# Performance work log

Measured on AMD Instinct MI355X. Metric: run time of the kernel, lower is better.

The kernel has to match this reference:

```python
import jax, jax.numpy as jnp
import numpy as np

N = 100000   # nodes
E = 1600000  # edges
D = 128      # input feature dim
H = 128      # hidden dim
C = 40       # output classes


def _gcn_conv(x, W, b, src, dst, norm):
    # PyG GCNConv: h = x @ W; out_i = sum_j (d_i^-1/2 d_j^-1/2) h_j over in-edges,
    # including self-loops, then + bias. norm = deg^-1/2 with self-loop-augmented degree.
    h = x @ W                                    # [N, H]
    coef = norm[src] * norm[dst]                 # [E]
    agg = jax.ops.segment_sum(h[src] * coef[:, None], dst, num_segments=N)
    agg = agg + h * (norm * norm)[:, None]       # self-loop term
    return agg + b


def setup_inputs() -> dict:
    key = jax.random.key(0)
    ks = jax.random.split(key, 12)
    x = jax.random.normal(ks[0], (N, D), dtype=jnp.float32)
    edge_index = jax.random.randint(ks[1], (2, E), 0, N, dtype=jnp.int64)

    def lin(k, fan_in, fan_out):
        s = 1.0 / np.sqrt(fan_in)
        return jax.random.uniform(k, (fan_in, fan_out), jnp.float32, -s, s)

    return {
        "x": x,
        "edge_index": edge_index,
        "W1": lin(ks[2], D, H), "b1": jnp.zeros((H,), jnp.float32),
        "W2": lin(ks[3], H, H), "b2": jnp.zeros((H,), jnp.float32),
        "W3": lin(ks[4], H, H), "b3": jnp.zeros((H,), jnp.float32),
        "Wp1": lin(ks[5], H, H), "bp1": jnp.zeros((H,), jnp.float32),
        "Wp2": lin(ks[6], H, C), "bp2": jnp.zeros((C,), jnp.float32),
    }


def reference(x, edge_index, W1, b1, W2, b2, W3, b3, Wp1, bp1, Wp2, bp2):
    src, dst = edge_index[0], edge_index[1]
    # degree with self-loops (GCNConv adds self-loops by default)
    deg = jax.ops.segment_sum(jnp.ones((E,), jnp.float32), dst, num_segments=N) + 1.0
    norm = jax.lax.rsqrt(deg)                    # deg^-1/2

    h = x
    for W, b in ((W1, b1), (W2, b2), (W3, b3)):
        h = _gcn_conv(h, W, b, src, dst, norm)
        h = jax.nn.relu(h)
        # dropout is a no-op at inference / rate 0

    h = h @ Wp1 + bp1
    h = h @ Wp2 + bp2
    return jax.nn.log_softmax(h, axis=1)
```

## Files before the change

### kernel.cpp

```cpp
#include <hip/hip_runtime.h>
#include <hip/hip_bf16.h>
#include <math.h>


#define DH 128
#define NC 40
#define BN 128
#define MAXNB 1024
#define CAP 2560
#define CH 4096
#define SP 136

typedef __attribute__((ext_vector_type(8))) short bf16x8;
typedef __attribute__((ext_vector_type(4))) float f32x4;

__device__ __forceinline__ unsigned short f2bf(float f) {
    unsigned u = __float_as_uint(f);
    unsigned r = (u + 0x7fffu + ((u >> 16) & 1u)) >> 16;
    return (unsigned short)r;
}
__device__ __forceinline__ unsigned pack2(float lo, float hi) {
    return (unsigned)f2bf(lo) | ((unsigned)f2bf(hi) << 16);
}


__global__ __launch_bounds__(256) void init_bpos(unsigned* __restrict__ bpos, int NB) {
    int i = blockIdx.x * 256 + threadIdx.x;
    if (i < NB) bpos[i] = (unsigned)i * CAP;
}


__global__ __launch_bounds__(256) void bucket_scatter(const int* __restrict__ src,
                                                      const int* __restrict__ dst, int E,
                                                      unsigned* __restrict__ bpos,
                                                      unsigned* __restrict__ ebuf) {
    __shared__ unsigned hist[MAXNB];
    __shared__ unsigned gbase[MAXNB];
    __shared__ unsigned lim[MAXNB];
    __shared__ unsigned cur[MAXNB];
    int tid = threadIdx.x;
    int e0 = blockIdx.x * CH;
    int nE = min(CH, E - e0);

    for (int i = tid; i < MAXNB; i += 256) { hist[i] = 0; cur[i] = 0; }
    __syncthreads();
    for (int i = tid; i < nE; i += 256)
        atomicAdd(&hist[(unsigned)dst[e0 + i] >> 7], 1u);
    __syncthreads();
    for (int i = tid; i < MAXNB; i += 256) {
        unsigned h = hist[i];
        if (h) {
            unsigned o = atomicAdd(&bpos[i], h);
            gbase[i] = o;
            lim[i] = min(o + h, (unsigned)(i + 1) * CAP);
        }
    }
    __syncthreads();
    for (int i = tid; i < nE; i += 256) {
        int s = src[e0 + i];
        int d = dst[e0 + i];
        unsigned b = (unsigned)d >> 7;
        unsigned p = gbase[b] + atomicAdd(&cur[b], 1u);
        if (p < lim[b]) ebuf[p] = ((unsigned)s << 7) | ((unsigned)d & 127u);
    }
}


__global__ __launch_bounds__(256) void bucket_degfill(const unsigned* __restrict__ ebuf,
                                                      const unsigned* __restrict__ bpos,
                                                      unsigned* __restrict__ cnt,
                                                      float* __restrict__ nrm,
                                                      unsigned* __restrict__ offN,
                                                      unsigned* __restrict__ dh,
                                                      int* __restrict__ csr, int N) {
    __shared__ unsigned h[BN], lb[BN], cur[BN];
    __shared__ int lcsr[CAP];
    __shared__ unsigned dhh[256];
    __shared__ unsigned tot;

    int b = blockIdx.x, tid = threadIdx.x;
    unsigned ebase = (unsigned)b * CAP;
    unsigned used = min(bpos[b] - ebase, (unsigned)CAP);

    if (tid < BN) { h[tid] = 0; cur[tid] = 0; }
    dhh[tid] = 0;
    if (tid == 0) tot = 0;
    __syncthreads();

    for (unsigned i = tid; i < used; i += 256)
        atomicAdd(&h[ebuf[ebase + i] & 127u], 1u);
    __syncthreads();

    if (tid < BN) {
        unsigned m = h[tid];
        lb[tid] = m ? atomicAdd(&tot, m) : 0u;
    }
    __syncthreads();

    for (unsigned i = tid; i < used; i += 256) {
        unsigned v = ebuf[ebase + i];
        unsigned nl = v & 127u;
        unsigned r = atomicAdd(&cur[nl], 1u);
        lcsr[lb[nl] + r] = (int)(v >> 7);
    }

    if (tid < BN) {
        int node = b * BN + tid;
        if (node < N) {
            unsigned m = h[tid];
            cnt[node] = m;
            nrm[node] = rsqrtf((float)m + 1.0f);
            offN[node] = ebase + lb[tid];
            atomicAdd(&dhh[min(m, 255u)], 1u);
        }
    }
    __syncthreads();

    for (unsigned i = tid; i < used; i += 256)
        csr[ebase + i] = lcsr[i];
    if (dhh[tid]) atomicAdd(&dh[tid], dhh[tid]);
}


__global__ __launch_bounds__(256) void deg_scatter(const unsigned* __restrict__ cnt, int N,
                                                   const unsigned* __restrict__ dh,
                                                   unsigned* __restrict__ binpos,
                                                   const unsigned* __restrict__ offN,
                                                   int* __restrict__ perm,
                                                   unsigned* __restrict__ pd2) {
    __shared__ unsigned hh[256], base[256], cur[256], sdh[256], sns[256];
    int t = threadIdx.x;
    hh[t] = 0; cur[t] = 0; sdh[t] = dh[t];
    __syncthreads();
    unsigned ns = 0;
    for (int d = t + 1; d < 256; ++d) ns += sdh[d];
    sns[t] = ns;
    int i = blockIdx.x * 256 + t;
    unsigned d = 0;
    if (i < N) { d = min(cnt[i], 255u); atomicAdd(&hh[d], 1u); }
    __syncthreads();
    if (hh[t]) base[t] = sns[t] + atomicAdd(&binpos[t], hh[t]);
    __syncthreads();
    if (i < N) {
        unsigned r = atomicAdd(&cur[d], 1u);
        unsigned idx = base[d] + r;
        perm[idx] = i;
        pd2[idx] = (offN[i] << 9) | min(cnt[i], 511u);
    }
}


__global__ __launch_bounds__(256) void prep_w(const float* __restrict__ W1,
                                              const float* __restrict__ W2,
                                              const float* __restrict__ W3,
                                              const float* __restrict__ Wp1,
                                              const float* __restrict__ bp1,
                                              const float* __restrict__ Wp2,
                                              const float* __restrict__ bp2,
                                              unsigned short* __restrict__ Wt,
                                              unsigned short* __restrict__ Wft,
                                              float* __restrict__ bfh) {
    int id = blockIdx.x * 256 + threadIdx.x;
    if (id < 3 * DH * DH) {
        int l = id >> 14, r = id & (DH * DH - 1);
        int k = r >> 7, n = r & 127;
        const float* W = (l == 0) ? W1 : (l == 1) ? W2 : W3;
        Wt[l * DH * DH + n * DH + k] = f2bf(W[k * DH + n]);
    } else if (id < 3 * DH * DH + 48 * DH) {
        int o = id - 3 * DH * DH;
        int c = o >> 7, k = o & 127;
        float acc = 0.f;
        if (c < NC)
            for (int j = 0; j < DH; ++j) acc += Wp1[k * DH + j] * Wp2[j * NC + c];
        Wft[c * DH + k] = f2bf(acc);
    } else if (id < 3 * DH * DH + 48 * DH + 48) {
        int c = id - 3 * DH * DH - 48 * DH;
        float acc = 0.f;
        if (c < NC) {
            acc = bp2[c];
            for (int j = 0; j < DH; ++j) acc += bp1[j] * Wp2[j * NC + c];
        }
        bfh[c] = acc;
    }
}


__global__ __launch_bounds__(256) void gemm_mfma_f32(const float* __restrict__ X,
                                                     const unsigned short* __restrict__ Wt,
                                                     const float* __restrict__ nrm,
                                                     unsigned short* __restrict__ outb,
                                                     int nrows) {
    const int tid = threadIdx.x;
    const int wave = tid >> 6;
    const int lane = tid & 63;
    const int m = lane & 15;
    const int quad = lane >> 4;
    const int rbase = blockIdx.x * 128 + wave * 32;

    union U8 { bf16x8 v; unsigned u[4]; };

    f32x4 acc[2][8];
#pragma unroll
    for (int rt = 0; rt < 2; ++rt)
#pragma unroll
        for (int ct = 0; ct < 8; ++ct) acc[rt][ct] = (f32x4){0.f, 0.f, 0.f, 0.f};

#pragma unroll
    for (int kt = 0; kt < 4; ++kt) {
        const int kof = kt * 32 + quad * 8;
        bf16x8 a[2], b[8];
#pragma unroll
        for (int rt = 0; rt < 2; ++rt) {
            int r = rbase + rt * 16 + m;
            r = (r < nrows) ? r : (nrows - 1);
            const float* p = X + (size_t)r * DH + kof;
            float4 u0 = *(const float4*)p;
            float4 u1 = *(const float4*)(p + 4);
            U8 t;
            t.u[0] = pack2(u0.x, u0.y);
            t.u[1] = pack2(u0.z, u0.w);
            t.u[2] = pack2(u1.x, u1.y);
            t.u[3] = pack2(u1.z, u1.w);
            a[rt] = t.v;
        }
#pragma unroll
        for (int ct = 0; ct < 8; ++ct)
            b[ct] = *(const bf16x8*)(Wt + (ct * 16 + m) * DH + kof);
#pragma unroll
        for (int rt = 0; rt < 2; ++rt)
#pragma unroll
            for (int ct = 0; ct < 8; ++ct)
                acc[rt][ct] = __builtin_amdgcn_mfma_f32_16x16x32_bf16(a[rt], b[ct], acc[rt][ct], 0, 0, 0);
    }

#pragma unroll
    for (int rt = 0; rt < 2; ++rt)
#pragma unroll
        for (int reg = 0; reg < 4; ++reg) {
            int r = rbase + rt * 16 + quad * 4 + reg;
            if (r < nrows) {
                float s = nrm[r];
#pragma unroll
                for (int ct = 0; ct < 8; ++ct)
                    outb[(size_t)r * DH + ct * 16 + m] = f2bf(acc[rt][ct][reg] * s);
            }
        }
}


__device__ __forceinline__ void bf8_add(float* acc, uint4 v) {
    acc[0] += __uint_as_float(v.x << 16);
    acc[1] += __uint_as_float(v.x & 0xffff0000u);
    acc[2] += __uint_as_float(v.y << 16);
    acc[3] += __uint_as_float(v.y & 0xffff0000u);
    acc[4] += __uint_as_float(v.z << 16);
    acc[5] += __uint_as_float(v.z & 0xffff0000u);
    acc[6] += __uint_as_float(v.w << 16);
    acc[7] += __uint_as_float(v.w & 0xffff0000u);
}

__device__ __forceinline__ void gather_phase(const uint4* __restrict__ Abf,
                                             const int* __restrict__ csr,
                                             const unsigned* __restrict__ pd2,
                                             const int* __restrict__ perm,
                                             const float* __restrict__ bias,
                                             unsigned short (*sA)[SP],
                                             int* snode, float* snrm, int N) {
    const int tid = threadIdx.x;
    const int g = tid >> 4;
    const int lane = tid & 15;
    const int idx = blockIdx.x * 16 + g;
    if (idx < N) {
        const unsigned pd = pd2[idx];
        const unsigned o = pd >> 9;
        const unsigned d = pd & 511u;
        const int node = perm[idx];

        float acc[8];
        {
            uint4 v = Abf[(size_t)node * 16 + lane];
            acc[0] = __uint_as_float(v.x << 16);
            acc[1] = __uint_as_float(v.x & 0xffff0000u);
            acc[2] = __uint_as_float(v.y << 16);
            acc[3] = __uint_as_float(v.y & 0xffff0000u);
            acc[4] = __uint_as_float(v.z << 16);
            acc[5] = __uint_as_float(v.z & 0xffff0000u);
            acc[6] = __uint_as_float(v.w << 16);
            acc[7] = __uint_as_float(v.w & 0xffff0000u);
        }

        unsigned e = 0;
        for (; e + 4 <= d; e += 4) {
            int s0 = csr[o + e + 0];
            int s1 = csr[o + e + 1];
            int s2 = csr[o + e + 2];
            int s3 = csr[o + e + 3];
            uint4 v0 = Abf[(size_t)s0 * 16 + lane];
            uint4 v1 = Abf[(size_t)s1 * 16 + lane];
            uint4 v2 = Abf[(size_t)s2 * 16 + lane];
            uint4 v3 = Abf[(size_t)s3 * 16 + lane];
            bf8_add(acc, v0);
            bf8_add(acc, v1);
            bf8_add(acc, v2);
            bf8_add(acc, v3);
        }
        for (; e < d; ++e) {
            int s = csr[o + e];
            uint4 v = Abf[(size_t)s * 16 + lane];
            bf8_add(acc, v);
        }

        float nm = rsqrtf((float)d + 1.0f);
        if (lane == 0) { snode[g] = node; snrm[g] = nm; }
        float4 b0 = *(const float4*)(bias + lane * 8);
        float4 b1 = *(const float4*)(bias + lane * 8 + 4);
        uint4 ov;
        ov.x = pack2(fmaxf(acc[0] * nm + b0.x, 0.f), fmaxf(acc[1] * nm + b0.y, 0.f));
        ov.y = pack2(fmaxf(acc[2] * nm + b0.z, 0.f), fmaxf(acc[3] * nm + b0.w, 0.f));
        ov.z = pack2(fmaxf(acc[4] * nm + b1.x, 0.f), fmaxf(acc[5] * nm + b1.y, 0.f));
        ov.w = pack2(fmaxf(acc[6] * nm + b1.z, 0.f), fmaxf(acc[7] * nm + b1.w, 0.f));
        *(uint4*)&sA[g][lane * 8] = ov;
    }
    __syncthreads();
}


__global__ __launch_bounds__(256) void agg_gemm(const uint4* __restrict__ Abf,
                                                const int* __restrict__ csr,
                                                const unsigned* __restrict__ pd2,
                                                const int* __restrict__ perm,
                                                const float* __restrict__ bias,
                                                const unsigned short* __restrict__ Wt,
                                                unsigned short* __restrict__ outb, int N) {
    __shared__ unsigned short sA[16][SP];
    __shared__ int snode[16];
    __shared__ float snrm[16];
    gather_phase(Abf, csr, pd2, perm, bias, sA, snode, snrm, N);

    const int tid = threadIdx.x;
    const int wave = tid >> 6;
    const int l64 = tid & 63;
    const int m = l64 & 15;
    const int quad = l64 >> 4;

    f32x4 acc[2];
    acc[0] = (f32x4){0.f, 0.f, 0.f, 0.f};
    acc[1] = (f32x4){0.f, 0.f, 0.f, 0.f};

#pragma unroll
    for (int kt = 0; kt < 4; ++kt) {
        const int kof = kt * 32 + quad * 8;
        bf16x8 a = *(const bf16x8*)&sA[m][kof];
#pragma unroll
        for (int c2 = 0; c2 < 2; ++c2) {
            const int ct = wave * 2 + c2;
            bf16x8 b = *(const bf16x8*)(Wt + (ct * 16 + m) * DH + kof);
            acc[c2] = __builtin_amdgcn_mfma_f32_16x16x32_bf16(a, b, acc[c2], 0, 0, 0);
        }
    }

#pragma unroll
    for (int reg = 0; reg < 4; ++reg) {
        int idx = blockIdx.x * 16 + quad * 4 + reg;
        if (idx < N) {
            int r = snode[quad * 4 + reg];
            float s = snrm[quad * 4 + reg];
#pragma unroll
            for (int c2 = 0; c2 < 2; ++c2)
                outb[(size_t)r * DH + (wave * 2 + c2) * 16 + m] = f2bf(acc[c2][reg] * s);
        }
    }
}


__global__ __launch_bounds__(256) void agg_head(const uint4* __restrict__ Abf,
                                                const int* __restrict__ csr,
                                                const unsigned* __restrict__ pd2,
                                                const int* __restrict__ perm,
                                                const float* __restrict__ bias,
                                                const unsigned short* __restrict__ Wft,
                                                const float* __restrict__ bfh,
                                                float* __restrict__ out, int N) {
    __shared__ unsigned short sA[16][SP];
    __shared__ int snode[16];
    __shared__ float snrm[16];
    gather_phase(Abf, csr, pd2, perm, bias, sA, snode, snrm, N);

    const int tid = threadIdx.x;
    if (tid >= 64) return;
    const int m = tid & 15;
    const int quad = tid >> 4;

    f32x4 acc[3];
#pragma unroll
    for (int ct = 0; ct < 3; ++ct) acc[ct] = (f32x4){0.f, 0.f, 0.f, 0.f};

#pragma unroll
    for (int kt = 0; kt < 4; ++kt) {
        const int kof = kt * 32 + quad * 8;
        bf16x8 a = *(const bf16x8*)&sA[m][kof];
#pragma unroll
        for (int ct = 0; ct < 3; ++ct) {
            bf16x8 b = *(const bf16x8*)(Wft + (ct * 16 + m) * DH + kof);
            acc[ct] = __builtin_amdgcn_mfma_f32_16x16x32_bf16(a, b, acc[ct], 0, 0, 0);
        }
    }

    float bias0 = bfh[m];
    float bias1 = bfh[16 + m];
    float bias2 = bfh[32 + m];

#pragma unroll
    for (int reg = 0; reg < 4; ++reg) {
        float v0 = acc[0][reg] + bias0;
        float v1 = acc[1][reg] + bias1;
        float v2 = (m < 8) ? (acc[2][reg] + bias2) : -1e30f;
        float mx = fmaxf(fmaxf(v0, v1), v2);
#pragma unroll
        for (int dlt = 1; dlt < 16; dlt <<= 1) mx = fmaxf(mx, __shfl_xor(mx, dlt));
        float s = __expf(v0 - mx) + __expf(v1 - mx) + ((m < 8) ? __expf(v2 - mx) : 0.f);
#pragma unroll
        for (int dlt = 1; dlt < 16; dlt <<= 1) s += __shfl_xor(s, dlt);
        float ls = mx + __logf(s);
        int idx = blockIdx.x * 16 + quad * 4 + reg;
        if (idx < N) {
            int r = snode[quad * 4 + reg];
            out[(size_t)r * NC + m] = v0 - ls;
            out[(size_t)r * NC + 16 + m] = v1 - ls;
            if (m < 8) out[(size_t)r * NC + 32 + m] = v2 - ls;
        }
    }
}


extern "C" void kernel_launch(void* const* d_in, const int* in_sizes, int n_in,
                              void* d_out, int out_size, void* d_ws, size_t ws_size,
                              hipStream_t stream) {
    const float* x   = (const float*)d_in[0];
    const int*   ei  = (const int*)d_in[1];
    const float* W1  = (const float*)d_in[2];
    const float* b1  = (const float*)d_in[3];
    const float* W2  = (const float*)d_in[4];
    const float* b2  = (const float*)d_in[5];
    const float* W3  = (const float*)d_in[6];
    const float* b3  = (const float*)d_in[7];
    const float* Wp1 = (const float*)d_in[8];
    const float* bp1 = (const float*)d_in[9];
    const float* Wp2 = (const float*)d_in[10];
    const float* bp2 = (const float*)d_in[11];
    float* out = (float*)d_out;

    const int N = in_sizes[0] / DH;
    const int E = in_sizes[1] / 2;
    const int* src = ei;
    const int* dst = ei + E;
    const int NB = (N + BN - 1) / BN;

    char* w = (char*)d_ws;
    unsigned short* Ab  = (unsigned short*)w; w += (size_t)N * DH * 2;
    unsigned short* Bb  = (unsigned short*)w; w += (size_t)N * DH * 2;
    int*      csr    = (int*)w;      w += (size_t)NB * CAP * 4;
    unsigned* ebuf   = (unsigned*)w; w += (size_t)NB * CAP * 4;
    unsigned* dh     = (unsigned*)w; w += 256 * 4;
    unsigned* binpos = (unsigned*)w; w += 256 * 4;
    unsigned* bpos   = (unsigned*)w; w += MAXNB * 4;
    unsigned* cnt    = (unsigned*)w; w += (size_t)N * 4;
    float*    nrm    = (float*)w;    w += (size_t)N * 4;
    unsigned* offN   = (unsigned*)w; w += (size_t)N * 4;
    unsigned* pd2    = (unsigned*)w; w += (size_t)((N + 31) & ~31) * 4;
    int*      perm   = (int*)w;      w += (size_t)((N + 31) & ~31) * 4;
    unsigned short* Wt  = (unsigned short*)w; w += 3 * DH * DH * 2;
    unsigned short* Wft = (unsigned short*)w; w += 48 * DH * 2;
    float*    bfh    = (float*)w;    w += 64 * 4;

    const int gC = (E + CH - 1) / CH;
    const int gN = (N + 255) / 256;

    hipMemsetAsync(dh, 0, 256 * 4 + 256 * 4, stream);
    init_bpos     <<<(NB + 255) / 256, 256, 0, stream>>>(bpos, NB);
    bucket_scatter<<<gC, 256, 0, stream>>>(src, dst, E, bpos, ebuf);
    bucket_degfill<<<NB, 256, 0, stream>>>(ebuf, bpos, cnt, nrm, offN, dh, csr, N);
    deg_scatter   <<<gN, 256, 0, stream>>>(cnt, N, dh, binpos, offN, perm, pd2);
    prep_w<<<(3 * DH * DH + 48 * DH + 48 + 255) / 256, 256, 0, stream>>>(
        W1, W2, W3, Wp1, bp1, Wp2, bp2, Wt, Wft, bfh);

    const int gG = (N + 127) / 128;
    const int gF = (N + 15) / 16;

    gemm_mfma_f32<<<gG, 256, 0, stream>>>(x, Wt, nrm, Ab, N);
    agg_gemm<<<gF, 256, 0, stream>>>((const uint4*)Ab, csr, pd2, perm, b1,
                                     Wt + DH * DH, Bb, N);
    agg_gemm<<<gF, 256, 0, stream>>>((const uint4*)Bb, csr, pd2, perm, b2,
                                     Wt + 2 * DH * DH, Ab, N);
    agg_head<<<gF, 256, 0, stream>>>((const uint4*)Ab, csr, pd2, perm, b3,
                                     Wft, bfh, out, N);
}
```

Baseline: 399.1 us.

## Vectorize bucketing loads, shuffle-broadcast CSR indices in gather, raise occupancy bounds

The bucket scatter and degree-fill kernels now read edge and bucket data as 128-bit vectors, and the CSR write-back is done in int4 chunks. In the gather phase, each 16-lane group loads up to 64 neighbor indices cooperatively and broadcasts them with shuffles, replacing the repeated scalar CSR loads per edge. Launch bounds on the aggregation kernels request 8 blocks per SM, which may push the compiler to limit registers. The aims are fewer memory transactions and more latency hiding, at the cost of shuffle overhead and possible register spills. The int4 loads also assume each chunk's base offset is 16-byte aligned.

```diff
diff --git a/kernel.cpp b/kernel.cpp
--- a/kernel.cpp
+++ b/kernel.cpp
@@ -41,10 +41,18 @@
     int tid = threadIdx.x;
     int e0 = blockIdx.x * CH;
     int nE = min(CH, E - e0);
+    int nE4 = nE & ~3;
 
     for (int i = tid; i < MAXNB; i += 256) { hist[i] = 0; cur[i] = 0; }
     __syncthreads();
-    for (int i = tid; i < nE; i += 256)
+    for (int i = tid * 4; i < nE4; i += 1024) {
+        int4 dv = *(const int4*)(dst + e0 + i);
+        atomicAdd(&hist[(unsigned)dv.x >> 7], 1u);
+        atomicAdd(&hist[(unsigned)dv.y >> 7], 1u);
+        atomicAdd(&hist[(unsigned)dv.z >> 7], 1u);
+        atomicAdd(&hist[(unsigned)dv.w >> 7], 1u);
+    }
+    for (int i = nE4 + tid; i < nE; i += 256)
         atomicAdd(&hist[(unsigned)dst[e0 + i] >> 7], 1u);
     __syncthreads();
     for (int i = tid; i < MAXNB; i += 256) {
@@ -56,7 +64,31 @@
         }
     }
     __syncthreads();
-    for (int i = tid; i < nE; i += 256) {
+    for (int i = tid * 4; i < nE4; i += 1024) {
+        int4 sv = *(const int4*)(src + e0 + i);
+        int4 dv = *(const int4*)(dst + e0 + i);
+        {
+            unsigned b = (unsigned)dv.x >> 7;
+            unsigned p = gbase[b] + atomicAdd(&cur[b], 1u);
+            if (p < lim[b]) ebuf[p] = ((unsigned)sv.x << 7) | ((unsigned)dv.x & 127u);
+        }
+        {
+            unsigned b = (unsigned)dv.y >> 7;
+            unsigned p = gbase[b] + atomicAdd(&cur[b], 1u);
+            if (p < lim[b]) ebuf[p] = ((unsigned)sv.y << 7) | ((unsigned)dv.y & 127u);
+        }
+        {
+            unsigned b = (unsigned)dv.z >> 7;
+            unsigned p = gbase[b] + atomicAdd(&cur[b], 1u);
+            if (p < lim[b]) ebuf[p] = ((unsigned)sv.z << 7) | ((unsigned)dv.z & 127u);
+        }
+        {
+            unsigned b = (unsigned)dv.w >> 7;
+            unsigned p = gbase[b] + atomicAdd(&cur[b], 1u);
+            if (p < lim[b]) ebuf[p] = ((unsigned)sv.w << 7) | ((unsigned)dv.w & 127u);
+        }
+    }
+    for (int i = nE4 + tid; i < nE; i += 256) {
         int s = src[e0 + i];
         int d = dst[e0 + i];
         unsigned b = (unsigned)d >> 7;
@@ -81,13 +113,21 @@
     int b = blockIdx.x, tid = threadIdx.x;
     unsigned ebase = (unsigned)b * CAP;
     unsigned used = min(bpos[b] - ebase, (unsigned)CAP);
+    unsigned used4 = used & ~3u;
 
     if (tid < BN) { h[tid] = 0; cur[tid] = 0; }
     dhh[tid] = 0;
     if (tid == 0) tot = 0;
     __syncthreads();
 
-    for (unsigned i = tid; i < used; i += 256)
+    for (unsigned i = tid * 4; i < used4; i += 1024) {
+        uint4 v = *(const uint4*)(ebuf + ebase + i);
+        atomicAdd(&h[v.x & 127u], 1u);
+        atomicAdd(&h[v.y & 127u], 1u);
+        atomicAdd(&h[v.z & 127u], 1u);
+        atomicAdd(&h[v.w & 127u], 1u);
+    }
+    for (unsigned i = used4 + tid; i < used; i += 256)
         atomicAdd(&h[ebuf[ebase + i] & 127u], 1u);
     __syncthreads();
 
@@ -97,7 +137,30 @@
     }
     __syncthreads();
 
-    for (unsigned i = tid; i < used; i += 256) {
+    for (unsigned i = tid * 4; i < used4; i += 1024) {
+        uint4 v = *(const uint4*)(ebuf + ebase + i);
+        {
+            unsigned nl = v.x & 127u;
+            unsigned r = atomicAdd(&cur[nl], 1u);
+            lcsr[lb[nl] + r] = (int)(v.x >> 7);
+        }
+        {
+            unsigned nl = v.y & 127u;
+            unsigned r = atomicAdd(&cur[nl], 1u);
+            lcsr[lb[nl] + r] = (int)(v.y >> 7);
+        }
+        {
+            unsigned nl = v.z & 127u;
+            unsigned r = atomicAdd(&cur[nl], 1u);
+            lcsr[lb[nl] + r] = (int)(v.z >> 7);
+        }
+        {
+            unsigned nl = v.w & 127u;
+            unsigned r = atomicAdd(&cur[nl], 1u);
+            lcsr[lb[nl] + r] = (int)(v.w >> 7);
+        }
+    }
+    for (unsigned i = used4 + tid; i < used; i += 256) {
         unsigned v = ebuf[ebase + i];
         unsigned nl = v & 127u;
         unsigned r = atomicAdd(&cur[nl], 1u);
@@ -116,7 +179,9 @@
     }
     __syncthreads();
 
-    for (unsigned i = tid; i < used; i += 256)
+    for (unsigned i = tid * 4; i < used4; i += 1024)
+        *(int4*)(csr + ebase + i) = *(const int4*)&lcsr[i];
+    for (unsigned i = used4 + tid; i < used; i += 256)
         csr[ebase + i] = lcsr[i];
     if (dhh[tid]) atomicAdd(&dh[tid], dhh[tid]);
 }
@@ -276,6 +341,12 @@
         const unsigned d = pd & 511u;
         const int node = perm[idx];
 
+        int i0 = 0, i1 = 0, i2 = 0, i3 = 0;
+        if ((unsigned)lane < d)      i0 = csr[o + lane];
+        if ((unsigned)(16 + lane) < d) i1 = csr[o + 16 + lane];
+        if ((unsigned)(32 + lane) < d) i2 = csr[o + 32 + lane];
+        if ((unsigned)(48 + lane) < d) i3 = csr[o + 48 + lane];
+
         float acc[8];
         {
             uint4 v = Abf[(size_t)node * 16 + lane];
@@ -289,12 +360,16 @@
             acc[7] = __uint_as_float(v.w & 0xffff0000u);
         }
 
+        const unsigned dl = min(d, 64u);
+        const int sb = g << 4;
         unsigned e = 0;
-        for (; e + 4 <= d; e += 4) {
-            int s0 = csr[o + e + 0];
-            int s1 = csr[o + e + 1];
-            int s2 = csr[o + e + 2];
-            int s3 = csr[o + e + 3];
+        for (; e + 4 <= dl; e += 4) {
+            int rsel = (e < 16) ? i0 : (e < 32) ? i1 : (e < 48) ? i2 : i3;
+            int bb = sb + (int)(e & 15u);
+            int s0 = __shfl(rsel, bb + 0);
+            int s1 = __shfl(rsel, bb + 1);
+            int s2 = __shfl(rsel, bb + 2);
+            int s3 = __shfl(rsel, bb + 3);
             uint4 v0 = Abf[(size_t)s0 * 16 + lane];
             uint4 v1 = Abf[(size_t)s1 * 16 + lane];
             uint4 v2 = Abf[(size_t)s2 * 16 + lane];
@@ -303,6 +378,12 @@
             bf8_add(acc, v1);
             bf8_add(acc, v2);
             bf8_add(acc, v3);
+        }
+        for (; e < dl; ++e) {
+            int rsel = (e < 16) ? i0 : (e < 32) ? i1 : (e < 48) ? i2 : i3;
+            int s = __shfl(rsel, sb + (int)(e & 15u));
+            uint4 v = Abf[(size_t)s * 16 + lane];
+            bf8_add(acc, v);
         }
         for (; e < d; ++e) {
             int s = csr[o + e];
@@ -325,13 +406,13 @@
 }
 
 
-__global__ __launch_bounds__(256) void agg_gemm(const uint4* __restrict__ Abf,
-                                                const int* __restrict__ csr,
-                                                const unsigned* __restrict__ pd2,
-                                                const int* __restrict__ perm,
-                                                const float* __restrict__ bias,
-                                                const unsigned short* __restrict__ Wt,
-                                                unsigned short* __restrict__ outb, int N) {
+__global__ __launch_bounds__(256, 8) void agg_gemm(const uint4* __restrict__ Abf,
+                                                   const int* __restrict__ csr,
+                                                   const unsigned* __restrict__ pd2,
+                                                   const int* __restrict__ perm,
+                                                   const float* __restrict__ bias,
+                                                   const unsigned short* __restrict__ Wt,
+                                                   unsigned short* __restrict__ outb, int N) {
     __shared__ unsigned short sA[16][SP];
     __shared__ int snode[16];
     __shared__ float snrm[16];
@@ -373,14 +454,14 @@
 }
 
 
-__global__ __launch_bounds__(256) void agg_head(const uint4* __restrict__ Abf,
-                                                const int* __restrict__ csr,
-                                                const unsigned* __restrict__ pd2,
-                                                const int* __restrict__ perm,
-                                                const float* __restrict__ bias,
-                                                const unsigned short* __restrict__ Wft,
-                                                const float* __restrict__ bfh,
-                                                float* __restrict__ out, int N) {
+__global__ __launch_bounds__(256, 8) void agg_head(const uint4* __restrict__ Abf,
+                                                   const int* __restrict__ csr,
+                                                   const unsigned* __restrict__ pd2,
+                                                   const int* __restrict__ perm,
+                                                   const float* __restrict__ bias,
+                                                   const unsigned short* __restrict__ Wft,
+                                                   const float* __restrict__ bfh,
+                                                   float* __restrict__ out, int N) {
     __shared__ unsigned short sA[16][SP];
     __shared__ int snode[16];
     __shared__ float snrm[16];
```

Measured after the change: 380.1 us. 1.05x faster.
